# Optimization experiments

Hardware: AMD Instinct MI355X
Metric: run time of the kernel (lower is better)

## Reference

```python
import jax, jax.numpy as jnp
import numpy as np

B, T, P = 16, 200, 100          # batch, timesteps, MAX_CODE_LEN paths
EMB = 100                        # per-table embedding dim
D = 3 * EMB                      # concatenated path-context dim = 300
NODE_VOCAB = 20000 + 2
PATH_VOCAB = 50000 + 2
SKILL = 30                       # self.skill_n
Q = 50                           # questions (rnn_first_part width)
OUT = 50                         # output_dim


def setup_inputs() -> dict:
    key = jax.random.key(0)
    ks = jax.random.split(key, 14)
    lin = lambda k, fi, fo: jax.random.uniform(k, (fi, fo), jnp.float32, -1.0, 1.0) / np.sqrt(fi)
    vec = lambda k, fi, fo: jax.random.uniform(k, (fo,), jnp.float32, -1.0, 1.0) / np.sqrt(fi)
    return {
        "x_float": jax.random.normal(ks[0], (B, T, Q), jnp.float32),
        "c2v_idx": jax.random.randint(ks[1], (B, T, P, 3), 0, NODE_VOCAB, jnp.int32),
        "embed_nodes": jax.random.normal(ks[2], (NODE_VOCAB, EMB), jnp.float32),
        "embed_paths": jax.random.normal(ks[3], (PATH_VOCAB, EMB), jnp.float32),
        "W_trans": lin(ks[4], D, D), "b_trans": vec(ks[5], D, D),
        "W_att": lin(ks[6], D, 1), "b_att": vec(ks[7], D, 1),
        "W_skill": lin(ks[8], D, SKILL), "b_skill": vec(ks[9], D, SKILL),
        "W_kc": lin(ks[10], Q, SKILL) + 0.15, "b_kc": vec(ks[11], Q, SKILL),
        "W_pred": lin(ks[12], SKILL, OUT), "b_pred": vec(ks[13], SKILL, OUT),
    }


def reference(x_float, c2v_idx, embed_nodes, embed_paths, W_trans, b_trans,
              W_att, b_att, W_skill, b_skill, W_kc, b_kc, W_pred, b_pred):
    # gather three embeddings per path triple  -> [B,T,P,100] each
    start_e = embed_nodes[c2v_idx[..., 0]]
    path_e = embed_paths[c2v_idx[..., 1]]
    end_e = embed_nodes[c2v_idx[..., 2]]
    full_embed = jnp.concatenate([start_e, end_e, path_e], axis=-1)   # [B,T,P,300]

    # path transformation + attention scores
    transformed = jnp.tanh(full_embed @ W_trans + b_trans)            # [B,T,P,300]
    context_w = transformed @ W_att + b_att                           # [B,T,P,1]
    # NOTE: original uses nn.Softmax(dim=1) -> softmax over the TIME axis
    attn = jax.nn.softmax(context_w, axis=1)                          # [B,T,P,1]
    code_vectors = jnp.sum(full_embed * attn, axis=2)                 # [B,T,300]

    kc_mask = jax.nn.sigmoid(x_float @ W_kc + b_kc)                   # [B,T,30]
    out = code_vectors @ W_skill + b_skill                            # [B,T,30]
    res2 = out * (kc_mask >= 0.5).astype(out.dtype)                   # hard-gated skills
    res = jax.nn.sigmoid(res2 @ W_pred + b_pred)                      # [B,T,50]
    return (res, res2, kc_mask, attn)
```

## Files before the change

kernel.cpp:

```cpp
#include <hip/hip_runtime.h>
#include <hip/hip_bf16.h>
#include <math.h>

#define Bdim 16
#define Tdim 200
#define Pdim 100
#define EMB  100
#define Ddim 300
#define SKILL 30
#define Qdim 50
#define OUTD 50

#define OFF_RES   0
#define OFF_RES2  (Bdim*Tdim*OUTD)
#define OFF_KC    (OFF_RES2 + Bdim*Tdim*SKILL)
#define OFF_ATTN  (OFF_KC + Bdim*Tdim*SKILL)

typedef __bf16 bf16x8 __attribute__((ext_vector_type(8)));
typedef __bf16 bf16x4 __attribute__((ext_vector_type(4)));
typedef float  f32x4  __attribute__((ext_vector_type(4)));

#define BM    128
#define KPAD  320
#define WROWS 352
#define ASTR  312
#define TPB   512
#define ESW   32
#define ESSTR 36

#define NROWS (Bdim*Tdim*Pdim)
#define EN_ELEMS (20002*EMB)
#define EP_ELEMS (50002*EMB)

#define WBT_BYTES ((size_t)WROWS*KPAD*2)
#define ENB_BYTES ((size_t)EN_ELEMS*2)
#define EPB_BYTES ((size_t)EP_ELEMS*2)
#define ES_BYTES  ((size_t)NROWS*ESW*4)
#define WS_NEED   (WBT_BYTES+ENB_BYTES+EPB_BYTES+ES_BYTES)

__device__ __forceinline__ float fast_tanh(float x) {
    float t = __expf(2.0f * x);
    return 1.0f - 2.0f * __builtin_amdgcn_rcpf(t + 1.0f);
}
__device__ __forceinline__ float sigmoidf_(float z) {
    return 1.f / (1.f + expf(-z));
}

__global__ __launch_bounds__(256) void prep_wbt_kernel(
    const float* __restrict__ Wt, const float* __restrict__ Wsk,
    __bf16* __restrict__ wbt)
{
    int id = blockIdx.x * 256 + threadIdx.x;
    if (id >= WROWS * KPAD) return;
    int j = id / KPAD, k = id - j * KPAD;
    float v = 0.0f;
    if (j < KPAD) {
        if (j < Ddim && k < Ddim) v = Wt[k * Ddim + j];
    } else {
        int s = j - KPAD;
        if (s < SKILL && k < Ddim) v = Wsk[k * SKILL + s];
    }
    wbt[id] = (__bf16)v;
}

__global__ __launch_bounds__(256) void prep_tables_kernel(
    const float* __restrict__ en, const float* __restrict__ ep,
    __bf16* __restrict__ enb, __bf16* __restrict__ epb)
{
    int id = blockIdx.x * 256 + threadIdx.x;
    const int entot = EN_ELEMS / 4;
    const int total = entot + EP_ELEMS / 4;
    if (id >= total) return;
    const float* s; __bf16* d; int off;
    if (id < entot) { s = en; d = enb; off = id * 4; }
    else            { s = ep; d = epb; off = (id - entot) * 4; }
    float4 v = *(const float4*)(s + off);
    bf16x4 b = { (__bf16)v.x, (__bf16)v.y, (__bf16)v.z, (__bf16)v.w };
    *(bf16x4*)(d + off) = b;
}

template <bool WRITE_ES, bool BT>
__global__ __launch_bounds__(TPB, 4) void score_mfma_kernel(
    const int*    __restrict__ c2v,
    const float*  __restrict__ en,  const float*  __restrict__ ep,
    const __bf16* __restrict__ enb, const __bf16* __restrict__ epb,
    const __bf16* __restrict__ wbt,
    const float*  __restrict__ bt,
    const float*  __restrict__ wa,
    const float*  __restrict__ ba,
    float* __restrict__ scores,
    float* __restrict__ es_out)
{
    __shared__ __align__(16) __bf16 A_lds[BM * ASTR];
    __shared__ __align__(16) char   aux_lds[2048];
    int*  idx_lds = (int*)aux_lds;
    float (*red_lds)[BM] = (float (*)[BM])aux_lds;
    float* es_stage = (float*)A_lds;

    const int tid = threadIdx.x;
    const int m0  = blockIdx.x * BM;

    if (tid < BM * 3) idx_lds[tid] = c2v[(size_t)m0 * 3 + tid];
    __syncthreads();

    {
        const int r   = tid >> 2;
        const int sub = tid & 3;
        const int i0 = idx_lds[r * 3 + 0];
        const int i1 = idx_lds[r * 3 + 1];
        const int i2 = idx_lds[r * 3 + 2];
        __bf16* arow = &A_lds[r * ASTR];
        if (BT) {
            const __bf16* srcs[3] = { enb + (size_t)i0 * EMB,
                                      enb + (size_t)i2 * EMB,
                                      epb + (size_t)i1 * EMB };
            #pragma unroll
            for (int seg = 0; seg < 3; ++seg) {
                const __bf16* src = srcs[seg];
                bf16x4 v[7];
                #pragma unroll
                for (int k = 0; k < 7; ++k) {
                    int j = sub + 4 * k;
                    if (j < 25) v[k] = *(const bf16x4*)(src + j * 4);
                }
                #pragma unroll
                for (int k = 0; k < 7; ++k) {
                    int j = sub + 4 * k;
                    if (j < 25) *(bf16x4*)(arow + seg * 100 + j * 4) = v[k];
                }
            }
        } else {
            const float* srcs[3] = { en + (size_t)i0 * EMB,
                                     en + (size_t)i2 * EMB,
                                     ep + (size_t)i1 * EMB };
            #pragma unroll
            for (int seg = 0; seg < 3; ++seg) {
                const float* src = srcs[seg];
                float4 v[7];
                #pragma unroll
                for (int k = 0; k < 7; ++k) {
                    int j = sub + 4 * k;
                    if (j < 25) v[k] = *(const float4*)(src + j * 4);
                }
                #pragma unroll
                for (int k = 0; k < 7; ++k) {
                    int j = sub + 4 * k;
                    if (j < 25) {
                        float4 w = v[k];
                        bf16x4 b4 = { (__bf16)w.x, (__bf16)w.y, (__bf16)w.z, (__bf16)w.w };
                        *(bf16x4*)(arow + seg * 100 + j * 4) = b4;
                    }
                }
            }
        }
        if (sub < 3) *(bf16x4*)(arow + 300 + sub * 4) = (bf16x4){};
    }
    __syncthreads();

    const int wid = tid >> 6, lane = tid & 63;
    const int wm = wid >> 2, wn = wid & 3;
    const int lr = lane & 15, lg = lane >> 4;
    const bool do_es = WRITE_ES && (wn < 2);

    f32x4 acc[4][5];
    #pragma unroll
    for (int mf = 0; mf < 4; ++mf)
        #pragma unroll
        for (int nf = 0; nf < 5; ++nf) acc[mf][nf] = (f32x4){0.f, 0.f, 0.f, 0.f};

    #pragma unroll
    for (int kt = 0; kt < 10; ++kt) {
        const int k0 = kt * 32;
        bf16x8 bfr[5];
        #pragma unroll
        for (int nf = 0; nf < 5; ++nf)
            bfr[nf] = *(const bf16x8*)&wbt[(size_t)(wn * 80 + nf * 16 + lr) * KPAD + k0 + lg * 8];
        bf16x8 af[4];
        #pragma unroll
        for (int mf = 0; mf < 4; ++mf) {
            bf16x8 a = *(const bf16x8*)&A_lds[(wm * 64 + mf * 16 + lr) * ASTR + k0 + lg * 8];
            if (kt == 9 && lg == 3) a = (bf16x8){};
            af[mf] = a;
        }
        #pragma unroll
        for (int mf = 0; mf < 4; ++mf)
            #pragma unroll
            for (int nf = 0; nf < 5; ++nf)
                acc[mf][nf] = __builtin_amdgcn_mfma_f32_16x16x32_bf16(
                    af[mf], bfr[nf], acc[mf][nf], 0, 0, 0);
    }

    f32x4 acc_es[4];
    #pragma unroll
    for (int mf = 0; mf < 4; ++mf) acc_es[mf] = (f32x4){0.f, 0.f, 0.f, 0.f};
    if (do_es) {
        #pragma unroll
        for (int kt = 0; kt < 10; ++kt) {
            const int k0 = kt * 32;
            bf16x8 bes = *(const bf16x8*)&wbt[(size_t)(KPAD + wn * 16 + lr) * KPAD + k0 + lg * 8];
            #pragma unroll
            for (int mf = 0; mf < 4; ++mf) {
                bf16x8 a = *(const bf16x8*)&A_lds[(wm * 64 + mf * 16 + lr) * ASTR + k0 + lg * 8];
                if (kt == 9 && lg == 3) a = (bf16x8){};
                acc_es[mf] = __builtin_amdgcn_mfma_f32_16x16x32_bf16(
                    a, bes, acc_es[mf], 0, 0, 0);
            }
        }
    }

    float btv[5], wav[5];
    #pragma unroll
    for (int nf = 0; nf < 5; ++nf) {
        int c = wn * 80 + nf * 16 + lr;
        bool ok = (c < Ddim);
        btv[nf] = ok ? bt[c] : 0.f;
        wav[nf] = ok ? wa[c] : 0.f;
    }
    float sred[4][4];
    #pragma unroll
    for (int mf = 0; mf < 4; ++mf) {
        #pragma unroll
        for (int i = 0; i < 4; ++i) {
            float s = 0.f;
            #pragma unroll
            for (int nf = 0; nf < 5; ++nf)
                s += fast_tanh(acc[mf][nf][i] + btv[nf]) * wav[nf];
            s += __shfl_xor(s, 1, 64);
            s += __shfl_xor(s, 2, 64);
            s += __shfl_xor(s, 4, 64);
            s += __shfl_xor(s, 8, 64);
            sred[mf][i] = s;
        }
    }
    __syncthreads();
    #pragma unroll
    for (int mf = 0; mf < 4; ++mf)
        #pragma unroll
        for (int i = 0; i < 4; ++i)
            if (lr == 0) red_lds[wn][wm * 64 + mf * 16 + lg * 4 + i] = sred[mf][i];
    if (do_es) {
        #pragma unroll
        for (int mf = 0; mf < 4; ++mf)
            #pragma unroll
            for (int i = 0; i < 4; ++i)
                es_stage[(wm * 64 + mf * 16 + lg * 4 + i) * ESSTR + wn * 16 + lr] = acc_es[mf][i];
    }
    __syncthreads();
    for (int r = tid; r < BM; r += TPB) {
        float s = ba[0] + red_lds[0][r] + red_lds[1][r] + red_lds[2][r] + red_lds[3][r];
        scores[m0 + r] = s;
    }
    if (WRITE_ES) {
        #pragma unroll
        for (int pos = tid; pos < BM * 8; pos += TPB) {
            int row = pos >> 3, c4 = pos & 7;
            float4 v = *(const float4*)&es_stage[row * ESSTR + c4 * 4];
            *(float4*)&es_out[(size_t)(m0 + row) * ESW + c4 * 4] = v;
        }
    }
}

__global__ __launch_bounds__(512) void softmax_time_kernel(float* __restrict__ a)
{
    __shared__ float s_lds[Tdim * Pdim];
    const int b = blockIdx.x, tid = threadIdx.x;
    float* base = a + (size_t)b * Tdim * Pdim;

    for (int i = tid; i < (Tdim * Pdim) / 4; i += 512)
        ((float4*)s_lds)[i] = ((const float4*)base)[i];
    __syncthreads();

    if (tid < Pdim) {
        const int p = tid;
        float m = -1e30f;
        for (int t = 0; t < Tdim; ++t) m = fmaxf(m, s_lds[t * Pdim + p]);
        float sum = 0.f;
        for (int t = 0; t < Tdim; ++t) {
            float e = expf(s_lds[t * Pdim + p] - m);
            s_lds[t * Pdim + p] = e;
            sum += e;
        }
        float inv = 1.f / sum;
        for (int t = 0; t < Tdim; ++t) s_lds[t * Pdim + p] *= inv;
    }
    __syncthreads();

    for (int i = tid; i < (Tdim * Pdim) / 4; i += 512)
        ((float4*)base)[i] = ((const float4*)s_lds)[i];
}

__global__ __launch_bounds__(512, 4) void cvpred5_kernel(
    const float* __restrict__ x,
    const float* __restrict__ ES,
    const float* __restrict__ attn,
    const float* __restrict__ bsk,
    const float* __restrict__ Wkc, const float* __restrict__ bkc,
    const float* __restrict__ Wpr, const float* __restrict__ bpr,
    float* __restrict__ res, float* __restrict__ res2, float* __restrict__ kcm)
{
    const int bt_i = blockIdx.x;
    const int tid  = threadIdx.x;

    __shared__ float es_lds[Pdim * 33];
    __shared__ float wkc_lds[Qdim * SKILL];
    __shared__ float wpr_lds[SKILL * OUTD];
    __shared__ float attn_lds[Pdim];
    __shared__ float x_lds[Qdim];
    __shared__ float zk_lds[SKILL], o_lds[SKILL], r2_lds[SKILL];

    {
        const float* src = ES + (size_t)bt_i * (Pdim * ESW);
        #pragma unroll
        for (int pos = tid; pos < Pdim * ESW; pos += 512)
            es_lds[(pos >> 5) * 33 + (pos & 31)] = src[pos];
    }
    for (int i = tid; i < (Qdim * SKILL) / 4; i += 512)
        ((float4*)wkc_lds)[i] = ((const float4*)Wkc)[i];
    for (int i = tid; i < (SKILL * OUTD) / 4; i += 512)
        ((float4*)wpr_lds)[i] = ((const float4*)Wpr)[i];
    if (tid < Pdim) attn_lds[tid] = attn[(size_t)bt_i * Pdim + tid];
    if (tid >= 128 && tid < 128 + Qdim) x_lds[tid - 128] = x[(size_t)bt_i * Qdim + tid - 128];
    __syncthreads();

    if (tid < 480) {
        const int s = tid >> 4, l = tid & 15;
        float o = 0.f;
        #pragma unroll
        for (int k = 0; k < 7; ++k) {
            int p = l + 16 * k;
            if (p < Pdim) o = fmaf(attn_lds[p], es_lds[p * 33 + s], o);
        }
        o += __shfl_xor(o, 8, 64);
        o += __shfl_xor(o, 4, 64);
        o += __shfl_xor(o, 2, 64);
        o += __shfl_xor(o, 1, 64);
        if (l == 0) o_lds[s] = o + bsk[s];
    }
    if (tid < 240) {
        const int s = tid >> 3, l = tid & 7;
        float zk = 0.f;
        #pragma unroll
        for (int j = 0; j < 7; ++j) {
            int q = l + 8 * j;
            if (q < Qdim) zk = fmaf(x_lds[q], wkc_lds[q * SKILL + s], zk);
        }
        zk += __shfl_xor(zk, 4, 64);
        zk += __shfl_xor(zk, 2, 64);
        zk += __shfl_xor(zk, 1, 64);
        if (l == 0) zk_lds[s] = zk + bkc[s];
    }
    __syncthreads();

    if (tid < SKILL) {
        float zk = zk_lds[tid];
        float r2 = (zk >= 0.f) ? o_lds[tid] : 0.f;
        kcm [(size_t)bt_i * SKILL + tid] = sigmoidf_(zk);
        res2[(size_t)bt_i * SKILL + tid] = r2;
        r2_lds[tid] = r2;
    }
    __syncthreads();

    if (tid < 400) {
        const int od = tid >> 3, l = tid & 7;
        float z = 0.f;
        #pragma unroll
        for (int j = 0; j < 4; ++j) {
            int s = l + 8 * j;
            if (s < SKILL) z = fmaf(r2_lds[s], wpr_lds[s * OUTD + od], z);
        }
        z += __shfl_xor(z, 4, 64);
        z += __shfl_xor(z, 2, 64);
        z += __shfl_xor(z, 1, 64);
        if (l == 0) res[(size_t)bt_i * OUTD + od] = sigmoidf_(z + bpr[od]);
    }
}

__global__ __launch_bounds__(512, 4) void cvpred4_kernel(
    const float*  __restrict__ x,
    const int*    __restrict__ c2v,
    const float*  __restrict__ en,
    const float*  __restrict__ ep,
    const float*  __restrict__ attn,
    const float* __restrict__ Wsk, const float* __restrict__ bsk,
    const float* __restrict__ Wkc, const float* __restrict__ bkc,
    const float* __restrict__ Wpr, const float* __restrict__ bpr,
    float* __restrict__ res, float* __restrict__ res2, float* __restrict__ kcm)
{
    const int bt_i = blockIdx.x;
    const int tid  = threadIdx.x;

    __shared__ float  wsk_lds[Ddim * SKILL];
    __shared__ float  wkc_lds[Qdim * SKILL];
    __shared__ float  wpr_lds[SKILL * OUTD];
    __shared__ int    idx_lds[Pdim * 3];
    __shared__ float  attn_lds[Pdim];
    __shared__ float  x_lds[Qdim];
    __shared__ float4 part_lds[6][76];
    __shared__ float  cv_lds[Ddim];
    __shared__ float  zk_lds[SKILL], o_lds[SKILL], r2_lds[SKILL];

    const int pg = tid / 75;
    const int ch = tid - pg * 75;

    for (int i = tid; i < (Ddim * SKILL) / 4; i += 512)
        ((float4*)wsk_lds)[i] = ((const float4*)Wsk)[i];
    for (int i = tid; i < (Qdim * SKILL) / 4; i += 512)
        ((float4*)wkc_lds)[i] = ((const float4*)Wkc)[i];
    for (int i = tid; i < (SKILL * OUTD) / 4; i += 512)
        ((float4*)wpr_lds)[i] = ((const float4*)Wpr)[i];
    if (tid < Pdim * 3) idx_lds[tid] = c2v[(size_t)bt_i * (Pdim * 3) + tid];
    if (tid >= 320 && tid < 320 + Pdim) attn_lds[tid - 320] = attn[(size_t)bt_i * Pdim + tid - 320];
    if (tid >= 448 && tid < 448 + Qdim) x_lds[tid - 448] = x[(size_t)bt_i * Qdim + tid - 448];
    __syncthreads();

    if (pg < 6) {
        const int seg = ch / 25, cq = ch - seg * 25;
        const float* tab = (seg == 2) ? ep : en;
        const int io = (seg == 0) ? 0 : (seg == 1) ? 2 : 1;
        int   ri[17];
        float rw[17];
        #pragma unroll
        for (int k = 0; k < 17; ++k) {
            int p = pg + 6 * k;
            bool ok = (p < Pdim);
            ri[k] = idx_lds[(ok ? p : 0) * 3 + io];
            rw[k] = ok ? attn_lds[p] : 0.f;
        }
        float4 acc = {0.f, 0.f, 0.f, 0.f};
        {
            float4 va[9];
            #pragma unroll
            for (int k = 0; k < 9; ++k)
                va[k] = *(const float4*)&tab[(size_t)ri[k] * EMB + cq * 4];
            #pragma unroll
            for (int k = 0; k < 9; ++k) {
                acc.x = fmaf(rw[k], va[k].x, acc.x);
                acc.y = fmaf(rw[k], va[k].y, acc.y);
                acc.z = fmaf(rw[k], va[k].z, acc.z);
                acc.w = fmaf(rw[k], va[k].w, acc.w);
            }
        }
        {
            float4 vb[8];
            #pragma unroll
            for (int k = 0; k < 8; ++k)
                vb[k] = *(const float4*)&tab[(size_t)ri[k + 9] * EMB + cq * 4];
            #pragma unroll
            for (int k = 0; k < 8; ++k) {
                acc.x = fmaf(rw[k + 9], vb[k].x, acc.x);
                acc.y = fmaf(rw[k + 9], vb[k].y, acc.y);
                acc.z = fmaf(rw[k + 9], vb[k].z, acc.z);
                acc.w = fmaf(rw[k + 9], vb[k].w, acc.w);
            }
        }
        part_lds[pg][ch] = acc;
    }
    __syncthreads();

    if (tid < 75) {
        float4 a0 = part_lds[0][tid], a1 = part_lds[1][tid];
        float4 a2 = part_lds[2][tid], a3 = part_lds[3][tid];
        float4 a4 = part_lds[4][tid], a5 = part_lds[5][tid];
        int c = tid * 4;
        cv_lds[c + 0] = a0.x + a1.x + a2.x + a3.x + a4.x + a5.x;
        cv_lds[c + 1] = a0.y + a1.y + a2.y + a3.y + a4.y + a5.y;
        cv_lds[c + 2] = a0.z + a1.z + a2.z + a3.z + a4.z + a5.z;
        cv_lds[c + 3] = a0.w + a1.w + a2.w + a3.w + a4.w + a5.w;
    }
    __syncthreads();

    if (tid < 480) {
        const int s = tid >> 4, l = tid & 15;
        float o = 0.f;
        #pragma unroll
        for (int j = 0; j < 19; ++j) {
            int c = l + 16 * j;
            if (c < Ddim) o = fmaf(cv_lds[c], wsk_lds[c * SKILL + s], o);
        }
        o += __shfl_xor(o, 8, 64);
        o += __shfl_xor(o, 4, 64);
        o += __shfl_xor(o, 2, 64);
        o += __shfl_xor(o, 1, 64);
        if (l == 0) o_lds[s] = o + bsk[s];
    }
    if (tid < 240) {
        const int s = tid >> 3, l = tid & 7;
        float zk = 0.f;
        #pragma unroll
        for (int j = 0; j < 7; ++j) {
            int q = l + 8 * j;
            if (q < Qdim) zk = fmaf(x_lds[q], wkc_lds[q * SKILL + s], zk);
        }
        zk += __shfl_xor(zk, 4, 64);
        zk += __shfl_xor(zk, 2, 64);
        zk += __shfl_xor(zk, 1, 64);
        if (l == 0) zk_lds[s] = zk + bkc[s];
    }
    __syncthreads();

    if (tid < SKILL) {
        float zk = zk_lds[tid];
        float r2 = (zk >= 0.f) ? o_lds[tid] : 0.f;
        kcm [(size_t)bt_i * SKILL + tid] = sigmoidf_(zk);
        res2[(size_t)bt_i * SKILL + tid] = r2;
        r2_lds[tid] = r2;
    }
    __syncthreads();

    if (tid < 400) {
        const int od = tid >> 3, l = tid & 7;
        float z = 0.f;
        #pragma unroll
        for (int j = 0; j < 4; ++j) {
            int s = l + 8 * j;
            if (s < SKILL) z = fmaf(r2_lds[s], wpr_lds[s * OUTD + od], z);
        }
        z += __shfl_xor(z, 4, 64);
        z += __shfl_xor(z, 2, 64);
        z += __shfl_xor(z, 1, 64);
        if (l == 0) res[(size_t)bt_i * OUTD + od] = sigmoidf_(z + bpr[od]);
    }
}

extern "C" void kernel_launch(void* const* d_in, const int* in_sizes, int n_in,
                              void* d_out, int out_size, void* d_ws, size_t ws_size,
                              hipStream_t stream)
{
    const float* x   = (const float*)d_in[0];
    const int*   c2v = (const int*)  d_in[1];
    const float* en  = (const float*)d_in[2];
    const float* ep  = (const float*)d_in[3];
    const float* Wt  = (const float*)d_in[4];
    const float* bt  = (const float*)d_in[5];
    const float* Wa  = (const float*)d_in[6];
    const float* ba  = (const float*)d_in[7];
    const float* Wsk = (const float*)d_in[8];
    const float* bsk = (const float*)d_in[9];
    const float* Wkc = (const float*)d_in[10];
    const float* bkc = (const float*)d_in[11];
    const float* Wpr = (const float*)d_in[12];
    const float* bpr = (const float*)d_in[13];

    float* out  = (float*)d_out;
    float* res  = out + OFF_RES;
    float* res2 = out + OFF_RES2;
    float* kcm  = out + OFF_KC;
    float* attn = out + OFF_ATTN;

    char* ws = (char*)d_ws;
    __bf16* wbt   = (__bf16*)ws;
    __bf16* enb   = (__bf16*)(ws + WBT_BYTES);
    __bf16* epb   = (__bf16*)(ws + WBT_BYTES + ENB_BYTES);
    float*  es_ws = (float*)(ws + WBT_BYTES + ENB_BYTES + EPB_BYTES);

    const bool use_es = ws_size >= WS_NEED;

    prep_wbt_kernel<<<(WROWS * KPAD + 255) / 256, 256, 0, stream>>>(Wt, Wsk, wbt);

    if (use_es) {
        prep_tables_kernel<<<((EN_ELEMS + EP_ELEMS) / 4 + 255) / 256, 256, 0, stream>>>(
            en, ep, enb, epb);
        score_mfma_kernel<true, true><<<NROWS / BM, TPB, 0, stream>>>(
            c2v, en, ep, enb, epb, wbt, bt, Wa, ba, attn, es_ws);
    } else {
        score_mfma_kernel<false, false><<<NROWS / BM, TPB, 0, stream>>>(
            c2v, en, ep, enb, epb, wbt, bt, Wa, ba, attn, es_ws);
    }

    softmax_time_kernel<<<Bdim, 512, 0, stream>>>(attn);

    if (use_es)
        cvpred5_kernel<<<Bdim * Tdim, 512, 0, stream>>>(
            x, es_ws, attn, bsk, Wkc, bkc, Wpr, bpr, res, res2, kcm);
    else
        cvpred4_kernel<<<Bdim * Tdim, 512, 0, stream>>>(
            x, c2v, en, ep, attn, Wsk, bsk, Wkc, bkc, Wpr, bpr, res, res2, kcm);
}
```

Before: 324.8 us.

## Merge prep kernels, parallelize time softmax per column, batch cvpred over timesteps

Merges the weight-transpose and table-conversion prep kernels into a single launch to cut one kernel launch. Rewrites the time-axis softmax so each (batch, path) column gets its own 64-thread wave with shuffle reductions, replacing 16 blocks that used only 100 active threads each. Changes the final prediction kernel to process four timesteps per block, amortizing the weight loads into shared memory at the cost of more LDS and lower occupancy. The softmax now reads with a strided, uncoalesced access pattern.

Result: faster. 307.5 us (-5.3%).

```diff
diff --git a/kernel.cpp b/kernel.cpp
--- a/kernel.cpp
+++ b/kernel.cpp
@@ -38,6 +38,11 @@
 #define ES_BYTES  ((size_t)NROWS*ESW*4)
 #define WS_NEED   (WBT_BYTES+ENB_BYTES+EPB_BYTES+ES_BYTES)
 
+#define WBT_IDS   (WROWS*KPAD)
+#define TAB_CHUNKS ((EN_ELEMS+EP_ELEMS)/4)
+
+#define BTPB  4
+
 __device__ __forceinline__ float fast_tanh(float x) {
     float t = __expf(2.0f * x);
     return 1.0f - 2.0f * __builtin_amdgcn_rcpf(t + 1.0f);
@@ -46,34 +51,31 @@
     return 1.f / (1.f + expf(-z));
 }
 
-__global__ __launch_bounds__(256) void prep_wbt_kernel(
+__global__ __launch_bounds__(256) void prep_all_kernel(
     const float* __restrict__ Wt, const float* __restrict__ Wsk,
-    __bf16* __restrict__ wbt)
+    const float* __restrict__ en, const float* __restrict__ ep,
+    __bf16* __restrict__ wbt, __bf16* __restrict__ enb, __bf16* __restrict__ epb,
+    int n_tab)
 {
     int id = blockIdx.x * 256 + threadIdx.x;
-    if (id >= WROWS * KPAD) return;
-    int j = id / KPAD, k = id - j * KPAD;
-    float v = 0.0f;
-    if (j < KPAD) {
-        if (j < Ddim && k < Ddim) v = Wt[k * Ddim + j];
-    } else {
-        int s = j - KPAD;
-        if (s < SKILL && k < Ddim) v = Wsk[k * SKILL + s];
-    }
-    wbt[id] = (__bf16)v;
-}
-
-__global__ __launch_bounds__(256) void prep_tables_kernel(
-    const float* __restrict__ en, const float* __restrict__ ep,
-    __bf16* __restrict__ enb, __bf16* __restrict__ epb)
-{
-    int id = blockIdx.x * 256 + threadIdx.x;
+    if (id < WBT_IDS) {
+        int j = id / KPAD, k = id - j * KPAD;
+        float v = 0.0f;
+        if (j < KPAD) {
+            if (j < Ddim && k < Ddim) v = Wt[k * Ddim + j];
+        } else {
+            int s = j - KPAD;
+            if (s < SKILL && k < Ddim) v = Wsk[k * SKILL + s];
+        }
+        wbt[id] = (__bf16)v;
+        return;
+    }
+    int c = id - WBT_IDS;
+    if (c >= n_tab) return;
     const int entot = EN_ELEMS / 4;
-    const int total = entot + EP_ELEMS / 4;
-    if (id >= total) return;
     const float* s; __bf16* d; int off;
-    if (id < entot) { s = en; d = enb; off = id * 4; }
-    else            { s = ep; d = epb; off = (id - entot) * 4; }
+    if (c < entot) { s = en; d = enb; off = c * 4; }
+    else           { s = ep; d = epb; off = (c - entot) * 4; }
     float4 v = *(const float4*)(s + off);
     bf16x4 b = { (__bf16)v.x, (__bf16)v.y, (__bf16)v.z, (__bf16)v.w };
     *(bf16x4*)(d + off) = b;
@@ -260,36 +262,42 @@
     }
 }
 
-__global__ __launch_bounds__(512) void softmax_time_kernel(float* __restrict__ a)
+__global__ __launch_bounds__(64) void softmax_time_kernel(float* __restrict__ a)
 {
-    __shared__ float s_lds[Tdim * Pdim];
-    const int b = blockIdx.x, tid = threadIdx.x;
-    float* base = a + (size_t)b * Tdim * Pdim;
-
-    for (int i = tid; i < (Tdim * Pdim) / 4; i += 512)
-        ((float4*)s_lds)[i] = ((const float4*)base)[i];
-    __syncthreads();
-
-    if (tid < Pdim) {
-        const int p = tid;
-        float m = -1e30f;
-        for (int t = 0; t < Tdim; ++t) m = fmaxf(m, s_lds[t * Pdim + p]);
-        float sum = 0.f;
-        for (int t = 0; t < Tdim; ++t) {
-            float e = expf(s_lds[t * Pdim + p] - m);
-            s_lds[t * Pdim + p] = e;
-            sum += e;
-        }
-        float inv = 1.f / sum;
-        for (int t = 0; t < Tdim; ++t) s_lds[t * Pdim + p] *= inv;
-    }
-    __syncthreads();
-
-    for (int i = tid; i < (Tdim * Pdim) / 4; i += 512)
-        ((float4*)base)[i] = ((const float4*)s_lds)[i];
-}
-
-__global__ __launch_bounds__(512, 4) void cvpred5_kernel(
+    const int b = blockIdx.x / Pdim;
+    const int p = blockIdx.x - b * Pdim;
+    const int lane = threadIdx.x;
+    const size_t base = (size_t)b * Tdim * Pdim + p;
+
+    float v[4];
+    float m = -1e30f;
+    #pragma unroll
+    for (int i = 0; i < 4; ++i) {
+        int t = lane + i * 64;
+        v[i] = (t < Tdim) ? a[base + (size_t)t * Pdim] : -1e30f;
+        m = fmaxf(m, v[i]);
+    }
+    #pragma unroll
+    for (int off = 32; off > 0; off >>= 1) m = fmaxf(m, __shfl_xor(m, off, 64));
+
+    float s = 0.f;
+    #pragma unroll
+    for (int i = 0; i < 4; ++i) {
+        int t = lane + i * 64;
+        if (t < Tdim) { v[i] = expf(v[i] - m); s += v[i]; }
+    }
+    #pragma unroll
+    for (int off = 32; off > 0; off >>= 1) s += __shfl_xor(s, off, 64);
+
+    const float inv = 1.f / s;
+    #pragma unroll
+    for (int i = 0; i < 4; ++i) {
+        int t = lane + i * 64;
+        if (t < Tdim) a[base + (size_t)t * Pdim] = v[i] * inv;
+    }
+}
+
+__global__ __launch_bounds__(512, 2) void cvpred6_kernel(
     const float* __restrict__ x,
     const float* __restrict__ ES,
     const float* __restrict__ attn,
@@ -298,80 +306,91 @@
     const float* __restrict__ Wpr, const float* __restrict__ bpr,
     float* __restrict__ res, float* __restrict__ res2, float* __restrict__ kcm)
 {
-    const int bt_i = blockIdx.x;
-    const int tid  = threadIdx.x;
-
-    __shared__ float es_lds[Pdim * 33];
+    const int bt0 = blockIdx.x * BTPB;
+    const int tid = threadIdx.x;
+
+    __shared__ float es_lds[BTPB * Pdim * 33];
     __shared__ float wkc_lds[Qdim * SKILL];
     __shared__ float wpr_lds[SKILL * OUTD];
-    __shared__ float attn_lds[Pdim];
-    __shared__ float x_lds[Qdim];
-    __shared__ float zk_lds[SKILL], o_lds[SKILL], r2_lds[SKILL];
+    __shared__ float attn_lds[BTPB * Pdim];
+    __shared__ float x_lds[BTPB * Qdim];
+    __shared__ float zk_lds[BTPB * SKILL], o_lds[BTPB * SKILL], r2_lds[BTPB * SKILL];
 
     {
-        const float* src = ES + (size_t)bt_i * (Pdim * ESW);
-        #pragma unroll
-        for (int pos = tid; pos < Pdim * ESW; pos += 512)
-            es_lds[(pos >> 5) * 33 + (pos & 31)] = src[pos];
+        const float* src = ES + (size_t)bt0 * (Pdim * ESW);
+        #pragma unroll
+        for (int pos = tid; pos < BTPB * Pdim * ESW; pos += 512) {
+            int row = pos >> 5, col = pos & 31;
+            es_lds[row * 33 + col] = src[pos];
+        }
     }
     for (int i = tid; i < (Qdim * SKILL) / 4; i += 512)
         ((float4*)wkc_lds)[i] = ((const float4*)Wkc)[i];
     for (int i = tid; i < (SKILL * OUTD) / 4; i += 512)
         ((float4*)wpr_lds)[i] = ((const float4*)Wpr)[i];
-    if (tid < Pdim) attn_lds[tid] = attn[(size_t)bt_i * Pdim + tid];
-    if (tid >= 128 && tid < 128 + Qdim) x_lds[tid - 128] = x[(size_t)bt_i * Qdim + tid - 128];
-    __syncthreads();
-
-    if (tid < 480) {
-        const int s = tid >> 4, l = tid & 15;
-        float o = 0.f;
-        #pragma unroll
-        for (int k = 0; k < 7; ++k) {
-            int p = l + 16 * k;
-            if (p < Pdim) o = fmaf(attn_lds[p], es_lds[p * 33 + s], o);
-        }
-        o += __shfl_xor(o, 8, 64);
-        o += __shfl_xor(o, 4, 64);
-        o += __shfl_xor(o, 2, 64);
-        o += __shfl_xor(o, 1, 64);
-        if (l == 0) o_lds[s] = o + bsk[s];
-    }
-    if (tid < 240) {
-        const int s = tid >> 3, l = tid & 7;
-        float zk = 0.f;
-        #pragma unroll
-        for (int j = 0; j < 7; ++j) {
-            int q = l + 8 * j;
-            if (q < Qdim) zk = fmaf(x_lds[q], wkc_lds[q * SKILL + s], zk);
-        }
-        zk += __shfl_xor(zk, 4, 64);
-        zk += __shfl_xor(zk, 2, 64);
-        zk += __shfl_xor(zk, 1, 64);
-        if (l == 0) zk_lds[s] = zk + bkc[s];
-    }
-    __syncthreads();
-
-    if (tid < SKILL) {
+    if (tid < BTPB * Pdim) attn_lds[tid] = attn[(size_t)bt0 * Pdim + tid];
+    if (tid >= 256 && tid < 256 + BTPB * Qdim)
+        x_lds[tid - 256] = x[(size_t)bt0 * Qdim + (tid - 256)];
+    __syncthreads();
+
+    #pragma unroll
+    for (int b = 0; b < BTPB; ++b) {
+        if (tid < 480) {
+            const int s = tid >> 4, l = tid & 15;
+            float o = 0.f;
+            #pragma unroll
+            for (int k = 0; k < 7; ++k) {
+                int p = l + 16 * k;
+                if (p < Pdim)
+                    o = fmaf(attn_lds[b * Pdim + p], es_lds[(b * Pdim + p) * 33 + s], o);
+            }
+            o += __shfl_xor(o, 8, 64);
+            o += __shfl_xor(o, 4, 64);
+            o += __shfl_xor(o, 2, 64);
+            o += __shfl_xor(o, 1, 64);
+            if (l == 0) o_lds[b * SKILL + s] = o + bsk[s];
+        }
+        if (tid < 240) {
+            const int s = tid >> 3, l = tid & 7;
+            float zk = 0.f;
+            #pragma unroll
+            for (int j = 0; j < 7; ++j) {
+                int q = l + 8 * j;
+                if (q < Qdim) zk = fmaf(x_lds[b * Qdim + q], wkc_lds[q * SKILL + s], zk);
+            }
+            zk += __shfl_xor(zk, 4, 64);
+            zk += __shfl_xor(zk, 2, 64);
+            zk += __shfl_xor(zk, 1, 64);
+            if (l == 0) zk_lds[b * SKILL + s] = zk + bkc[s];
+        }
+    }
+    __syncthreads();
+
+    if (tid < BTPB * SKILL) {
+        const int b = tid / SKILL, s = tid - b * SKILL;
         float zk = zk_lds[tid];
         float r2 = (zk >= 0.f) ? o_lds[tid] : 0.f;
-        kcm [(size_t)bt_i * SKILL + tid] = sigmoidf_(zk);
-        res2[(size_t)bt_i * SKILL + tid] = r2;
+        kcm [(size_t)(bt0 + b) * SKILL + s] = sigmoidf_(zk);
+        res2[(size_t)(bt0 + b) * SKILL + s] = r2;
         r2_lds[tid] = r2;
     }
     __syncthreads();
 
-    if (tid < 400) {
-        const int od = tid >> 3, l = tid & 7;
-        float z = 0.f;
-        #pragma unroll
-        for (int j = 0; j < 4; ++j) {
-            int s = l + 8 * j;
-            if (s < SKILL) z = fmaf(r2_lds[s], wpr_lds[s * OUTD + od], z);
-        }
-        z += __shfl_xor(z, 4, 64);
-        z += __shfl_xor(z, 2, 64);
-        z += __shfl_xor(z, 1, 64);
-        if (l == 0) res[(size_t)bt_i * OUTD + od] = sigmoidf_(z + bpr[od]);
+    #pragma unroll
+    for (int b = 0; b < BTPB; ++b) {
+        if (tid < 400) {
+            const int od = tid >> 3, l = tid & 7;
+            float z = 0.f;
+            #pragma unroll
+            for (int j = 0; j < 4; ++j) {
+                int s = l + 8 * j;
+                if (s < SKILL) z = fmaf(r2_lds[b * SKILL + s], wpr_lds[s * OUTD + od], z);
+            }
+            z += __shfl_xor(z, 4, 64);
+            z += __shfl_xor(z, 2, 64);
+            z += __shfl_xor(z, 1, 64);
+            if (l == 0) res[(size_t)(bt0 + b) * OUTD + od] = sigmoidf_(z + bpr[od]);
+        }
     }
 }
 
@@ -555,22 +574,22 @@
 
     const bool use_es = ws_size >= WS_NEED;
 
-    prep_wbt_kernel<<<(WROWS * KPAD + 255) / 256, 256, 0, stream>>>(Wt, Wsk, wbt);
-
-    if (use_es) {
-        prep_tables_kernel<<<((EN_ELEMS + EP_ELEMS) / 4 + 255) / 256, 256, 0, stream>>>(
-            en, ep, enb, epb);
+    const int n_tab = use_es ? TAB_CHUNKS : 0;
+    const int prep_ids = WBT_IDS + n_tab;
+    prep_all_kernel<<<(prep_ids + 255) / 256, 256, 0, stream>>>(
+        Wt, Wsk, en, ep, wbt, enb, epb, n_tab);
+
+    if (use_es)
         score_mfma_kernel<true, true><<<NROWS / BM, TPB, 0, stream>>>(
             c2v, en, ep, enb, epb, wbt, bt, Wa, ba, attn, es_ws);
-    } else {
+    else
         score_mfma_kernel<false, false><<<NROWS / BM, TPB, 0, stream>>>(
             c2v, en, ep, enb, epb, wbt, bt, Wa, ba, attn, es_ws);
-    }
-
-    softmax_time_kernel<<<Bdim, 512, 0, stream>>>(attn);
+
+    softmax_time_kernel<<<Bdim * Pdim, 64, 0, stream>>>(attn);
 
     if (use_es)
-        cvpred5_kernel<<<Bdim * Tdim, 512, 0, stream>>>(
+        cvpred6_kernel<<<(Bdim * Tdim) / BTPB, 512, 0, stream>>>(
             x, es_ws, attn, bsk, Wkc, bkc, Wpr, bpr, res, res2, kcm);
     else
         cvpred4_kernel<<<Bdim * Tdim, 512, 0, stream>>>(
```
